# Kernel tuning notes

Measured on AMD Instinct MI355X. Metric: run time of the kernel, lower is better.

Reference implementation:

```python
import jax, jax.numpy as jnp
import numpy as np

B = 128; DIM_IN = 3; MAX_CYCLE = 50; NODES = 18
T = MAX_CYCLE * NODES          # cycle_size = 900
F1, F2 = 32, 64                # stgcn_filters
NCLS = 3
N = B * T                      # nodes seen by GATv2 = 115200
E = 12 * N                     # edges (avg degree 12)
EPS = 1e-5


def setup_inputs() -> dict:
    key = jax.random.key(0)
    keys = iter(jax.random.split(key, 48))
    def p(shape, scale=0.05):
        return jax.random.normal(next(keys), shape, jnp.float32) * scale
    inp = {}
    inp["x"] = jax.random.normal(next(keys), (B, DIM_IN, T), jnp.float32)
    inp["edge_index"] = jax.random.randint(next(keys), (2, E), 0, N)
    def block(pfx, cin, c):
        inp[pfx + "_tc1_w"] = p((c, cin, 5)); inp[pfx + "_tc1_b"] = p((c,))
        inp[pfx + "_wl"] = p((c, c)); inp[pfx + "_bl"] = p((c,))
        inp[pfx + "_wr"] = p((c, c)); inp[pfx + "_br"] = p((c,))
        inp[pfx + "_att"] = p((c,)); inp[pfx + "_gbias"] = p((c,))
        inp[pfx + "_bn_g"] = jnp.ones((c,), jnp.float32)
        inp[pfx + "_bn_b"] = jnp.zeros((c,), jnp.float32)
        inp[pfx + "_tc2_w"] = p((c, c, 5)); inp[pfx + "_tc2_b"] = p((c,))
    block("b1", DIM_IN, F1)
    block("b2", F1, F2)
    inp["fc1_w"] = p((128, T * F2), 0.01); inp["fc1_b"] = p((128,))
    inp["hbn1_g"] = jnp.ones((128,), jnp.float32); inp["hbn1_b"] = jnp.zeros((128,), jnp.float32)
    inp["fc2_w"] = p((64, 128)); inp["fc2_b"] = p((64,))
    inp["hbn2_g"] = jnp.ones((64,), jnp.float32); inp["hbn2_b"] = jnp.zeros((64,), jnp.float32)
    inp["fc3_w"] = p((NCLS, 64)); inp["fc3_b"] = p((NCLS,))
    return inp


def _conv1d_same(x, w, b):
    # x: [B, Cin, T], w: [Cout, Cin, 5], 'same' padding (pad 2/2)
    y = jax.lax.conv_general_dilated(x, w, (1,), [(2, 2)],
                                     dimension_numbers=("NCH", "OIH", "NCH"))
    return y + b[None, :, None]


def _bn(h, g, b):
    # BatchNorm1d on [N, C] with batch statistics
    m = h.mean(0)
    v = h.var(0)
    return (h - m) * jax.lax.rsqrt(v + EPS) * g + b


def _gatv2(h, src, dst, wl, bl, wr, br, att, gbias):
    # PyG GATv2Conv, heads=1, negative_slope=0.2, self loops already in src/dst
    xl = h @ wl.T + bl            # source transform, also the message
    xr = h @ wr.T + br            # target transform
    e = jnp.dot(jax.nn.leaky_relu(xl[src] + xr[dst], 0.2), att)  # [E]
    m = jax.ops.segment_max(e, dst, num_segments=N)
    ex = jnp.exp(e - m[dst])
    s = jax.ops.segment_sum(ex, dst, num_segments=N)
    alpha = ex / s[dst]
    out = jax.ops.segment_sum(alpha[:, None] * xl[src], dst, num_segments=N)
    return out + gbias


def _block(x, src, dst, tc1_w, tc1_b, wl, bl, wr, br, att, gbias, bn_g, bn_b, tc2_w, tc2_b):
    x = jax.nn.relu(_conv1d_same(x, tc1_w, tc1_b))      # [B, C, T]
    C = tc1_w.shape[0]
    h = x.reshape(T * B, C)                             # torch .view(T*B, C) (raw row-major)
    h = jax.nn.relu(_gatv2(h, src, dst, wl, bl, wr, br, att, gbias))
    h = _bn(h, bn_g, bn_b)
    h = h.reshape(B, C, T)                              # torch .view(B, C, T)
    return jax.nn.relu(_conv1d_same(h, tc2_w, tc2_b))


def reference(x, edge_index,
              b1_tc1_w, b1_tc1_b, b1_wl, b1_bl, b1_wr, b1_br, b1_att, b1_gbias,
              b1_bn_g, b1_bn_b, b1_tc2_w, b1_tc2_b,
              b2_tc1_w, b2_tc1_b, b2_wl, b2_bl, b2_wr, b2_br, b2_att, b2_gbias,
              b2_bn_g, b2_bn_b, b2_tc2_w, b2_tc2_b,
              fc1_w, fc1_b, hbn1_g, hbn1_b, fc2_w, fc2_b, hbn2_g, hbn2_b, fc3_w, fc3_b):
    sl = jnp.arange(N, dtype=edge_index.dtype)          # PyG add_self_loops=True
    src = jnp.concatenate([edge_index[0], sl])
    dst = jnp.concatenate([edge_index[1], sl])
    h = _block(x, src, dst, b1_tc1_w, b1_tc1_b, b1_wl, b1_bl, b1_wr, b1_br,
               b1_att, b1_gbias, b1_bn_g, b1_bn_b, b1_tc2_w, b1_tc2_b)
    h = jax.nn.relu(h)                                  # extra relu on non-final block (dropout off)
    h = _block(h, src, dst, b2_tc1_w, b2_tc1_b, b2_wl, b2_bl, b2_wr, b2_br,
               b2_att, b2_gbias, b2_bn_g, b2_bn_b, b2_tc2_w, b2_tc2_b)
    h = h.reshape(B, F2 * T)
    h = jax.nn.relu(h @ fc1_w.T + fc1_b)
    h = _bn(h, hbn1_g, hbn1_b)
    h = jax.nn.relu(h @ fc2_w.T + fc2_b)
    h = _bn(h, hbn2_g, hbn2_b)
    logits = h @ fc3_w.T + fc3_b
    return (jax.nn.sigmoid(logits), logits)
```

## Files before the change

kernel.cpp:

```cpp
#include <hip/hip_runtime.h>
#include <hip/hip_bf16.h>

typedef __hip_bfloat16 bf16;
typedef __attribute__((ext_vector_type(8))) short s16x8;
typedef __attribute__((ext_vector_type(4))) float f32x4;
#define DEV static __device__ __forceinline__

DEV float b2f(bf16 v){ return __bfloat162float(v); }
DEV bf16  f2b(float v){ return __float2bfloat16(v); }
DEV int   is_f32(const void* gones){ return ((const unsigned int*)gones)[0] == 0x3F800000u ? 1 : 0; }
DEV float ldin(const void* p, int f32, int i){
    return f32 ? ((const float*)p)[i] : __bfloat162float(((const bf16*)p)[i]);
}
DEV void unpk(unsigned u, float& a, float& b){
    a = __uint_as_float(u << 16);
    b = __uint_as_float(u & 0xffff0000u);
}
DEV float lrelu(float t){ return fmaxf(t, 0.f) + 0.2f * fminf(t, 0.f); }
DEV unsigned short bfu(float v){ bf16 h = f2b(v); return *(unsigned short*)&h; }

constexpr int Bb  = 128;
constexpr int Tt  = 900;
constexpr int Nn  = Bb * Tt;
constexpr int Ee  = 12 * Nn;
constexpr int CAP = 48;
constexpr int NBK  = 256;
constexpr int NPB  = Nn / NBK;
constexpr int BCAP = 8192;
constexpr int WROWS = 96 + 1024 + 2048 + 4096;
constexpr int WTOT  = WROWS * 5;
constexpr int WBF   = 5120 + 10240 + 20480;
constexpr int WXT   = 2*32*32 + 64 + 2*64*64 + 128;

__global__ __launch_bounds__(256) void k_wprep(const void* wa, const void* wb_, const void* wc,
    const void* wd,
    const void* b1wl, const void* b1bl, const void* b1wr, const void* b1br,
    const void* b2wl, const void* b2bl, const void* b2wr, const void* b2br,
    const void* gones, float* __restrict__ wp, bf16* __restrict__ wbf,
    float* __restrict__ wx, int* __restrict__ gcur){
    const int f32 = is_f32(gones);
    if (blockIdx.x == 0 && threadIdx.x < NBK) gcur[threadIdx.x] = 0;
    int e = blockIdx.x * 256 + threadIdx.x;
    if (e < WTOT){
        int r = e / 5, k = e - r * 5;
        const void* src; int rb;
        if (r < 96)      { src = wa; rb = 0; }
        else if (r < 1120){ src = wb_; rb = 96; }
        else if (r < 3168){ src = wc; rb = 1120; }
        else             { src = wd; rb = 3168; }
        wp[r * 8 + k] = ldin(src, f32, (r - rb) * 5 + k);
    } else if (e < WTOT + WBF){
        int e2 = e - WTOT;
        const void* src; int kk, r;
        if (e2 < 5120)      { kk = e2 >> 10; r = e2 & 1023; src = wb_; }
        else if (e2 < 15360){ int e3 = e2 - 5120;  kk = e3 >> 11; r = e3 & 2047; src = wc; }
        else                { int e3 = e2 - 15360; kk = e3 >> 12; r = e3 & 4095; src = wd; }
        wbf[e2] = f2b(ldin(src, f32, r * 5 + kk));
    } else if (e < WTOT + WBF + WXT){
        int e3 = e - WTOT - WBF;
        float v;
        if      (e3 < 1024){ int t = e3;         int c = t >> 5, f = t & 31; v = ldin(b1wl, f32, f * 32 + c); }
        else if (e3 < 2048){ int t = e3 - 1024;  int c = t >> 5, f = t & 31; v = ldin(b1wr, f32, f * 32 + c); }
        else if (e3 < 2080)  v = ldin(b1bl, f32, e3 - 2048);
        else if (e3 < 2112)  v = ldin(b1br, f32, e3 - 2080);
        else if (e3 < 6208){ int t = e3 - 2112;  int c = t >> 6, f = t & 63; v = ldin(b2wl, f32, f * 64 + c); }
        else if (e3 < 10304){int t = e3 - 6208;  int c = t >> 6, f = t & 63; v = ldin(b2wr, f32, f * 64 + c); }
        else if (e3 < 10368) v = ldin(b2bl, f32, e3 - 10304);
        else                 v = ldin(b2br, f32, e3 - 10368);
        wx[e3] = v;
    }
}

__global__ __launch_bounds__(256) void k_bucket(const int* __restrict__ ei,
                                                int* __restrict__ gcur, int2* __restrict__ bkt){
    constexpr int TILE = 4096;
    const int base = blockIdx.x * TILE;
    const int tid = threadIdx.x;
    __shared__ int cnt[NBK];
    __shared__ int gbase[NBK];
    cnt[tid] = 0;
    __syncthreads();
    int es[16], er[16], eb[16], rk[16];
    #pragma unroll
    for (int k = 0; k < 16; ++k){
        int idx = base + k * 256 + tid;
        if (idx < Ee){
            es[k] = ei[idx];
            int d = ei[Ee + idx];
            eb[k] = d / NPB;
            er[k] = d - eb[k] * NPB;
            rk[k] = atomicAdd(&cnt[eb[k]], 1);
        } else eb[k] = -1;
    }
    __syncthreads();
    {
        int c = cnt[tid];
        gbase[tid] = (c > 0) ? atomicAdd(&gcur[tid], c) : 0;
    }
    __syncthreads();
    #pragma unroll
    for (int k = 0; k < 16; ++k){
        if (eb[k] >= 0){
            int slot = gbase[eb[k]] + rk[k];
            if (slot < BCAP)
                bkt[(size_t)eb[k] * BCAP + slot] = make_int2(er[k], es[k]);
        }
    }
}

__global__ __launch_bounds__(256) void k_csr2(const int2* __restrict__ bkt, const int* __restrict__ gcur,
                                              int* __restrict__ csr, int* __restrict__ cnt){
    const int b = blockIdx.x;
    const int n0 = b * NPB;
    __shared__ int lcnt[NPB];
    for (int i = threadIdx.x; i < NPB; i += 256) lcnt[i] = 0;
    __syncthreads();
    const int tot = min(gcur[b], BCAP);
    for (int i = threadIdx.x; i < tot; i += 256){
        int2 e = bkt[(size_t)b * BCAP + i];
        int p = atomicAdd(&lcnt[e.x], 1);
        if (p < CAP) csr[(size_t)(n0 + e.x) * CAP + p] = e.y;
    }
    __syncthreads();
    for (int i = threadIdx.x; i < NPB; i += 256) cnt[n0 + i] = lcnt[i];
}

template<bool EXT, int CIN, int COUT, bool BN>
__global__ __launch_bounds__(256) void k_conv(const void* __restrict__ x,
    const float* __restrict__ wp, int wbase,
    const void* __restrict__ bias, const float* __restrict__ scale, const float* __restrict__ shift,
    const void* __restrict__ gones, float* __restrict__ y)
{
    const int f32 = is_f32(gones);
    __shared__ alignas(16) float xs[CIN][132];
    const int b = blockIdx.x >> 3, t0 = (blockIdx.x & 7) * 128;
    const int tid = threadIdx.x;
    for (int i = tid; i < CIN * 132; i += 256){
        int ci = i / 132, tt = i % 132;
        int gt = t0 + tt - 2;
        float v = 0.f;
        if (gt >= 0 && gt < Tt){
            int idx = (b * CIN + ci) * Tt + gt;
            v = EXT ? ldin(x, f32, idx) : ((const float*)x)[idx];
            if (BN){
                int f = (ci * (Tt % CIN) + gt) % CIN;
                v = v * scale[f] + shift[f];
            }
        }
        xs[ci][tt] = v;
    }
    __syncthreads();
    constexpr int HALF = COUT / 2;
    constexpr int NT   = 256 / HALF;
    constexpr int NW   = 128 / (NT * 4);
    const int cop = tid / NT;
    const int tch = tid % NT;
    const int co = cop, co2 = cop + HALF;
    float acc[NW][2][4];
    #pragma unroll
    for (int iw = 0; iw < NW; ++iw)
        #pragma unroll
        for (int h = 0; h < 2; ++h)
            #pragma unroll
            for (int j = 0; j < 4; ++j) acc[iw][h][j] = 0.f;

    const float* w0p = wp + (size_t)(wbase + co  * CIN) * 8;
    const float* w1p = wp + (size_t)(wbase + co2 * CIN) * 8;
    float4 na = *(const float4*)w0p; float na4 = w0p[4];
    float4 nb = *(const float4*)w1p; float nb4 = w1p[4];
    for (int ci = 0; ci < CIN; ++ci){
        const float w0[5] = {na.x, na.y, na.z, na.w, na4};
        const float w1[5] = {nb.x, nb.y, nb.z, nb.w, nb4};
        if (ci + 1 < CIN){
            const float* p0 = w0p + (size_t)(ci + 1) * 8;
            const float* p1 = w1p + (size_t)(ci + 1) * 8;
            na = *(const float4*)p0; na4 = p0[4];
            nb = *(const float4*)p1; nb4 = p1[4];
        }
        #pragma unroll
        for (int iw = 0; iw < NW; ++iw){
            const int tl = tch * 4 + iw * NT * 4;
            float4 a  = *(const float4*)&xs[ci][tl];
            float4 bq = *(const float4*)&xs[ci][tl + 4];
            float xw[8] = {a.x,a.y,a.z,a.w,bq.x,bq.y,bq.z,bq.w};
            #pragma unroll
            for (int k = 0; k < 5; ++k)
                #pragma unroll
                for (int j = 0; j < 4; ++j){
                    acc[iw][0][j] = fmaf(xw[j + k], w0[k], acc[iw][0][j]);
                    acc[iw][1][j] = fmaf(xw[j + k], w1[k], acc[iw][1][j]);
                }
        }
    }
    const float bv0 = ldin(bias, f32, co), bv1 = ldin(bias, f32, co2);
    #pragma unroll
    for (int iw = 0; iw < NW; ++iw){
        const int t = t0 + tch * 4 + iw * NT * 4;
        if (t < Tt){
            float4 o0, o1;
            o0.x = fmaxf(acc[iw][0][0] + bv0, 0.f); o0.y = fmaxf(acc[iw][0][1] + bv0, 0.f);
            o0.z = fmaxf(acc[iw][0][2] + bv0, 0.f); o0.w = fmaxf(acc[iw][0][3] + bv0, 0.f);
            o1.x = fmaxf(acc[iw][1][0] + bv1, 0.f); o1.y = fmaxf(acc[iw][1][1] + bv1, 0.f);
            o1.z = fmaxf(acc[iw][1][2] + bv1, 0.f); o1.w = fmaxf(acc[iw][1][3] + bv1, 0.f);
            *(float4*)&y[(b * COUT + co ) * Tt + t] = o0;
            *(float4*)&y[(b * COUT + co2) * Tt + t] = o1;
        }
    }
}

template<int CIN, int COUT, bool BN>
__global__ __launch_bounds__(256) void k_convM(const float* __restrict__ x, const bf16* __restrict__ wbf,
    int wbase,
    const void* __restrict__ bias, const float* __restrict__ scale, const float* __restrict__ shift,
    const void* __restrict__ gones, float* __restrict__ y)
{
    const int f32 = is_f32(gones);
    constexpr int STR = CIN + 8;
    constexpr int CI2 = CIN / 2;
    __shared__ alignas(16) float smem[COUT * 132];
    unsigned short* xsT = (unsigned short*)smem;
    const int b = blockIdx.x >> 3, t0 = (blockIdx.x & 7) * 128;
    const int tid = threadIdx.x;
    for (int i = tid; i < CI2 * 128; i += 256){
        int ci2 = i >> 7, tt = i & 127;
        int gt = t0 + tt - 2;
        int ci = ci2 * 2;
        unsigned pack = 0;
        if (gt >= 0 && gt < Tt){
            float v0 = x[(b * CIN + ci) * Tt + gt];
            float v1 = x[(b * CIN + ci + 1) * Tt + gt];
            if (BN){
                int fa = (4 * ci + gt) & (CIN - 1), fb = (4 * ci + 4 + gt) & (CIN - 1);
                v0 = v0 * scale[fa] + shift[fa];
                v1 = v1 * scale[fb] + shift[fb];
            }
            pack = (unsigned)bfu(v0) | ((unsigned)bfu(v1) << 16);
        }
        *(unsigned*)&xsT[tt * STR + ci] = pack;
    }
    if (tid < CI2 * 4){
        int ci2 = tid >> 2, tt = 128 + (tid & 3);
        int gt = t0 + tt - 2;
        int ci = ci2 * 2;
        unsigned pack = 0;
        if (gt < Tt){
            float v0 = x[(b * CIN + ci) * Tt + gt];
            float v1 = x[(b * CIN + ci + 1) * Tt + gt];
            if (BN){
                int fa = (4 * ci + gt) & (CIN - 1), fb = (4 * ci + 4 + gt) & (CIN - 1);
                v0 = v0 * scale[fa] + shift[fa];
                v1 = v1 * scale[fb] + shift[fb];
            }
            pack = (unsigned)bfu(v0) | ((unsigned)bfu(v1) << 16);
        }
        *(unsigned*)&xsT[tt * STR + ci] = pack;
    }
    __syncthreads();
    const int lane = tid & 63, wid = tid >> 6;
    const int l15 = lane & 15, quad = lane >> 4;
    constexpr int MT  = COUT / 16;
    constexpr int NTP = 2 * MT;
    const int mt  = (MT == 4) ? wid : (wid & 1);
    const int ntb = (MT == 4) ? 0 : (wid >> 1) * NTP;
    const int co0 = mt * 16;
    f32x4 acc[NTP];
    #pragma unroll
    for (int nt = 0; nt < NTP; ++nt){ f32x4 z = {0.f, 0.f, 0.f, 0.f}; acc[nt] = z; }
    for (int kk = 0; kk < 5; ++kk){
        #pragma unroll
        for (int kb = 0; kb < CIN / 32; ++kb){
            s16x8 a = *(const s16x8*)&wbf[wbase + kk * (COUT * CIN) + (co0 + l15) * CIN + kb * 32 + quad * 8];
            #pragma unroll
            for (int nt = 0; nt < NTP; ++nt){
                s16x8 bf = *(const s16x8*)&xsT[((ntb + nt) * 16 + l15 + kk) * STR + kb * 32 + quad * 8];
                acc[nt] = __builtin_amdgcn_mfma_f32_16x16x32_bf16(a, bf, acc[nt], 0, 0, 0);
            }
        }
    }
    __syncthreads();
    #pragma unroll
    for (int nt = 0; nt < NTP; ++nt)
        #pragma unroll
        for (int r = 0; r < 4; ++r)
            smem[(co0 + quad * 4 + r) * 132 + (ntb + nt) * 16 + l15] = acc[nt][r];
    __syncthreads();
    for (int i = tid; i < COUT * 32; i += 256){
        int co = i >> 5, c4 = (i & 31) << 2;
        int t = t0 + c4;
        if (t < Tt){
            float4 o = *(float4*)&smem[co * 132 + c4];
            float bb = ldin(bias, f32, co);
            o.x = fmaxf(o.x + bb, 0.f); o.y = fmaxf(o.y + bb, 0.f);
            o.z = fmaxf(o.z + bb, 0.f); o.w = fmaxf(o.w + bb, 0.f);
            float* dst = &y[(b * COUT + co) * Tt + t];
            if (t + 3 < Tt) *(float4*)dst = o;
            else {
                float ov[4] = {o.x, o.y, o.z, o.w};
                for (int j = 0; j < 4 && t + j < Tt; ++j) dst[j] = ov[j];
            }
        }
    }
}

template<int C>
__global__ __launch_bounds__(256) void k_xlxr(const float* __restrict__ h,
    const float* __restrict__ wx, int wxoff,
    unsigned short* __restrict__ xlh, float* __restrict__ xr)
{
    constexpr int NB = 4096 / C;
    constexpr int HS = NB + 4;
    __shared__ alignas(16) float hT[C][HS];
    __shared__ alignas(16) float wlS[C * C];
    __shared__ alignas(16) float wrS[C * C];
    const int tid = threadIdx.x;
    const int n0 = blockIdx.x * NB;
    for (int i = tid; i < NB * C; i += 256){
        int n = i & (NB - 1), c = i / NB;
        hT[c][n] = h[(size_t)(n0 + n) * C + c];
    }
    const float* wl = wx + wxoff;
    const float* wr = wl + C * C;
    for (int i = tid; i < C * C; i += 256){
        wlS[i] = wl[i];
        wrS[i] = wr[i];
    }
    __syncthreads();
    const float* bl = wr + C * C;
    const float* br = bl + C;
    constexpr int FG = C / 4;
    const int fg = tid % FG, ng = tid / FG;
    const int nloc = ng * 4, floc = fg * 4;
    float blv[4], brv[4];
    #pragma unroll
    for (int j = 0; j < 4; ++j){ blv[j] = bl[floc + j]; brv[j] = br[floc + j]; }
    float accL[4][4], accR[4][4];
    #pragma unroll
    for (int i = 0; i < 4; ++i)
        #pragma unroll
        for (int j = 0; j < 4; ++j){ accL[i][j] = 0.f; accR[i][j] = 0.f; }
    #pragma unroll 4
    for (int c = 0; c < C; ++c){
        float4 hv = *(const float4*)&hT[c][nloc];
        float4 lv = *(const float4*)&wlS[c * C + floc];
        float4 rv = *(const float4*)&wrS[c * C + floc];
        float ha[4] = {hv.x,hv.y,hv.z,hv.w};
        float la[4] = {lv.x,lv.y,lv.z,lv.w};
        float ra[4] = {rv.x,rv.y,rv.z,rv.w};
        #pragma unroll
        for (int i = 0; i < 4; ++i)
            #pragma unroll
            for (int j = 0; j < 4; ++j){
                accL[i][j] = fmaf(ha[i], la[j], accL[i][j]);
                accR[i][j] = fmaf(ha[i], ra[j], accR[i][j]);
            }
    }
    #pragma unroll
    for (int i = 0; i < 4; ++i){
        size_t n = n0 + nloc + i;
        bf16 hb[4];
        hb[0] = f2b(accL[i][0] + blv[0]); hb[1] = f2b(accL[i][1] + blv[1]);
        hb[2] = f2b(accL[i][2] + blv[2]); hb[3] = f2b(accL[i][3] + blv[3]);
        *(ushort4*)&xlh[n * C + floc] = *(ushort4*)hb;
        float4 r;
        r.x = accR[i][0] + brv[0]; r.y = accR[i][1] + brv[1];
        r.z = accR[i][2] + brv[2]; r.w = accR[i][3] + brv[3];
        *(float4*)&xr[n * C + floc] = r;
    }
}

template<int L> DEV float rsumL(float v){
    #pragma unroll
    for (int s = L / 2; s > 0; s >>= 1) v += __shfl_xor(v, s, 64);
    return v;
}

template<int C, int FPL>
__global__ __launch_bounds__(256) void k_gat(const unsigned short* __restrict__ xlh,
    const float* __restrict__ xr,
    const int* __restrict__ csr, const int* __restrict__ cnt,
    const void* __restrict__ att, const void* __restrict__ gbias,
    const void* __restrict__ gones, float* __restrict__ out)
{
    const int f32 = is_f32(gones);
    constexpr int L   = C / FPL;
    constexpr int NPW = 64 / L;
    const int lane = threadIdx.x & 63, wid = threadIdx.x >> 6;
    const int sub = lane / L, fp = lane % L;
    const int node = (blockIdx.x * 4 + wid) * NPW + sub;
    const int f0 = FPL * fp;
    float xrv[FPL], attv[FPL];
    if constexpr (FPL == 4){
        float4 t = *(const float4*)&xr[(size_t)node * C + f0];
        xrv[0] = t.x; xrv[1] = t.y; xrv[2] = t.z; xrv[3] = t.w;
    } else {
        float2 t = *(const float2*)&xr[(size_t)node * C + f0];
        xrv[0] = t.x; xrv[1] = t.y;
    }
    #pragma unroll
    for (int i = 0; i < FPL; ++i) attv[i] = ldin(att, f32, f0 + i);
    const int deg = min(cnt[node], CAP);
    int degu = deg;
    degu = max(degu, __shfl_xor(degu, 32, 64));
    degu = max(degu, __shfl_xor(degu, 16, 64));

    auto loadv = [&](int s, float (&v)[FPL]){
        if constexpr (FPL == 4){
            uint2 u = *(const uint2*)&xlh[(size_t)s * C + f0];
            unpk(u.x, v[0], v[1]); unpk(u.y, v[2], v[3]);
        } else {
            unsigned u = *(const unsigned*)&xlh[(size_t)s * C + f0];
            unpk(u, v[0], v[1]);
        }
    };
    auto score = [&](const float (&v)[FPL]){
        float l = lrelu(v[0] + xrv[0]) * attv[0];
        #pragma unroll
        for (int i = 1; i < FPL; ++i) l = fmaf(lrelu(v[i] + xrv[i]), attv[i], l);
        return rsumL<L>(l);
    };

    float ssum, acc[FPL];
    {
        float v[FPL];
        loadv(node, v);
        float w = __expf(score(v));
        ssum = w;
        #pragma unroll
        for (int i = 0; i < FPL; ++i) acc[i] = w * v[i];
    }
    for (int j = 0; j < degu; j += 4){
        int4 s4 = *(const int4*)&csr[(size_t)node * CAP + j];
        const bool a0 = (j + 0 < deg), a1 = (j + 1 < deg), a2 = (j + 2 < deg), a3 = (j + 3 < deg);
        int s0 = a0 ? s4.x : node, s1 = a1 ? s4.y : node;
        int s2 = a2 ? s4.z : node, s3 = a3 ? s4.w : node;
        float v0[FPL], v1[FPL], v2[FPL], v3[FPL];
        loadv(s0, v0); loadv(s1, v1); loadv(s2, v2); loadv(s3, v3);
        float e0 = score(v0), e1 = score(v1), e2 = score(v2), e3 = score(v3);
        float w0 = a0 ? __expf(e0) : 0.f;
        float w1 = a1 ? __expf(e1) : 0.f;
        float w2 = a2 ? __expf(e2) : 0.f;
        float w3 = a3 ? __expf(e3) : 0.f;
        ssum += (w0 + w1) + (w2 + w3);
        #pragma unroll
        for (int i = 0; i < FPL; ++i)
            acc[i] += fmaf(w0, v0[i], w1 * v1[i]) + fmaf(w2, v2[i], w3 * v3[i]);
    }
    float inv = 1.f / ssum;
    if constexpr (FPL == 4){
        float4 o;
        o.x = fmaxf(fmaf(acc[0], inv, ldin(gbias, f32, f0)),     0.f);
        o.y = fmaxf(fmaf(acc[1], inv, ldin(gbias, f32, f0 + 1)), 0.f);
        o.z = fmaxf(fmaf(acc[2], inv, ldin(gbias, f32, f0 + 2)), 0.f);
        o.w = fmaxf(fmaf(acc[3], inv, ldin(gbias, f32, f0 + 3)), 0.f);
        *(float4*)&out[(size_t)node * C + f0] = o;
    } else {
        float2 o;
        o.x = fmaxf(fmaf(acc[0], inv, ldin(gbias, f32, f0)),     0.f);
        o.y = fmaxf(fmaf(acc[1], inv, ldin(gbias, f32, f0 + 1)), 0.f);
        *(float2*)&out[(size_t)node * C + f0] = o;
    }
}

template<int C>
__global__ __launch_bounds__(256) void k_bnstat1(const float* __restrict__ h, double* __restrict__ part){
    const int tid = threadIdx.x;
    double s1 = 0.0, s2 = 0.0;
    const int total = Nn * C;
    for (int idx = blockIdx.x * 256 + tid; idx < total; idx += 65536){
        float v = h[idx];
        s1 += v; s2 += (double)v * v;
    }
    __shared__ double r1[256], r2[256];
    r1[tid] = s1; r2[tid] = s2;
    __syncthreads();
    if (tid < C){
        double a = 0.0, b = 0.0;
        #pragma unroll
        for (int q = 0; q < 256 / C; ++q){ a += r1[tid + q * C]; b += r2[tid + q * C]; }
        part[blockIdx.x * 2 * C + tid]     = a;
        part[blockIdx.x * 2 * C + C + tid] = b;
    }
}

template<int C>
__global__ void k_bnstat2(const double* __restrict__ part, const void* __restrict__ g,
                          const void* __restrict__ b, const void* __restrict__ gones,
                          float* __restrict__ scale, float* __restrict__ shift){
    const int f32 = is_f32(gones);
    const int f = threadIdx.x;
    double s1 = 0.0, s2 = 0.0;
    for (int s = 0; s < 256; ++s){ s1 += part[s * 2 * C + f]; s2 += part[s * 2 * C + C + f]; }
    double mean = s1 / (double)Nn;
    double var  = s2 / (double)Nn - mean * mean;
    float sc = (float)((double)ldin(g, f32, f) / sqrt(var + 1e-5));
    float sh = ldin(b, f32, f) - (float)mean * sc;
    scale[f] = sc; shift[f] = sh;
}

__global__ __launch_bounds__(256) void k_fc1(const float* __restrict__ h, const void* __restrict__ w1,
                                             const void* __restrict__ gones, float* __restrict__ part){
    const int f32 = is_f32(gones);
    __shared__ alignas(16) float AT[32][136];
    __shared__ alignas(16) float BT[32][136];
    const int tid = threadIdx.x;
    const int blk = blockIdx.x;
    const int k0 = blk * 128;
    const int bg = tid >> 4, jg = tid & 15;
    const int row = tid >> 5, kk = tid & 31;
    float ar[16], br[16];
    #pragma unroll
    for (int q = 0; q < 16; ++q){
        int idx = (row + q * 8) * 57600 + k0 + kk;
        ar[q] = h[idx];
        br[q] = ldin(w1, f32, idx);
    }
    float acc[8][8];
    #pragma unroll
    for (int i = 0; i < 8; ++i)
        #pragma unroll
        for (int j = 0; j < 8; ++j) acc[i][j] = 0.f;
    for (int ch = 0; ch < 4; ++ch){
        __syncthreads();
        #pragma unroll
        for (int q = 0; q < 16; ++q){
            AT[kk][row + q * 8] = ar[q];
            BT[kk][row + q * 8] = br[q];
        }
        __syncthreads();
        if (ch < 3){
            const int kb = k0 + (ch + 1) * 32;
            #pragma unroll
            for (int q = 0; q < 16; ++q){
                int idx = (row + q * 8) * 57600 + kb + kk;
                ar[q] = h[idx];
                br[q] = ldin(w1, f32, idx);
            }
        }
        for (int k2 = 0; k2 < 32; ++k2){
            float4 a0 = *(const float4*)&AT[k2][bg * 8];
            float4 a1 = *(const float4*)&AT[k2][bg * 8 + 4];
            float4 c0 = *(const float4*)&BT[k2][jg * 8];
            float4 c1 = *(const float4*)&BT[k2][jg * 8 + 4];
            float av[8] = {a0.x,a0.y,a0.z,a0.w,a1.x,a1.y,a1.z,a1.w};
            float bv[8] = {c0.x,c0.y,c0.z,c0.w,c1.x,c1.y,c1.z,c1.w};
            #pragma unroll
            for (int i = 0; i < 8; ++i)
                #pragma unroll
                for (int j = 0; j < 8; ++j) acc[i][j] = fmaf(av[i], bv[j], acc[i][j]);
        }
    }
    #pragma unroll
    for (int i = 0; i < 8; ++i){
        int bb = bg * 8 + i;
        #pragma unroll
        for (int q = 0; q < 2; ++q){
            float4 o;
            o.x = acc[i][q*4+0]; o.y = acc[i][q*4+1]; o.z = acc[i][q*4+2]; o.w = acc[i][q*4+3];
            *(float4*)&part[blk * 16384 + bb * 128 + jg * 8 + q * 4] = o;
        }
    }
}

__global__ void k_fc1red1(const float* __restrict__ part, float* __restrict__ pr2){
    const int y = blockIdx.x >> 6;
    const int o = (blockIdx.x & 63) * 256 + threadIdx.x;
    const int sb0 = y * 57;
    const int sb1 = min(sb0 + 57, 450);
    float s = 0.f;
    for (int sb = sb0; sb < sb1; ++sb) s += part[(size_t)sb * 16384 + o];
    pr2[(size_t)y * 16384 + o] = s;
}

__global__ void k_fc1red2(const float* __restrict__ pr2, const void* __restrict__ bias,
                          const void* __restrict__ gones, float* __restrict__ out1){
    const int f32 = is_f32(gones);
    const int o = blockIdx.x * 256 + threadIdx.x;
    float s = ldin(bias, f32, o & 127);
    #pragma unroll
    for (int y = 0; y < 8; ++y) s += pr2[(size_t)y * 16384 + o];
    out1[o] = fmaxf(s, 0.f);
}

__global__ void k_hstat(const float* __restrict__ out1, const void* __restrict__ g1,
                        const void* __restrict__ b1, const void* __restrict__ gones,
                        float* __restrict__ sc, float* __restrict__ sh){
    const int f32 = is_f32(gones);
    const int f = threadIdx.x;
    double s1 = 0.0, s2 = 0.0;
    for (int r = 0; r < 128; ++r){ float v = out1[r * 128 + f]; s1 += v; s2 += (double)v * v; }
    double mean = s1 / 128.0, var = s2 / 128.0 - mean * mean;
    float s = (float)((double)ldin(g1, f32, f) / sqrt(var + 1e-5));
    sc[f] = s;
    sh[f] = ldin(b1, f32, f) - (float)mean * s;
}

__global__ __launch_bounds__(256) void k_fc2(const float* __restrict__ out1,
    const float* __restrict__ sc, const float* __restrict__ sh,
    const void* __restrict__ w2, const void* __restrict__ fb2,
    const void* __restrict__ gones, float* __restrict__ f2)
{
    const int f32 = is_f32(gones);
    __shared__ alignas(16) float hs[4 * 128];
    __shared__ alignas(16) float w2s[64 * 132];
    const int tid = threadIdx.x;
    const int b0 = blockIdx.x * 4;
    for (int i = tid; i < 512; i += 256){
        int f = i & 127;
        hs[i] = out1[b0 * 128 + i] * sc[f] + sh[f];
    }
    for (int i = tid; i < 8192; i += 256)
        w2s[(i >> 7) * 132 + (i & 127)] = ldin(w2, f32, i);
    __syncthreads();
    const int b = tid >> 6, o = tid & 63;
    float acc = ldin(fb2, f32, o);
    const float* hp = &hs[b * 128];
    const float* wq = &w2s[o * 132];
    #pragma unroll
    for (int k = 0; k < 128; k += 4){
        float4 hv = *(const float4*)&hp[k];
        float4 wv = *(const float4*)&wq[k];
        acc = fmaf(hv.x, wv.x, acc); acc = fmaf(hv.y, wv.y, acc);
        acc = fmaf(hv.z, wv.z, acc); acc = fmaf(hv.w, wv.w, acc);
    }
    f2[(b0 + b) * 64 + o] = fmaxf(acc, 0.f);
}

__global__ __launch_bounds__(256) void k_head2(const float* __restrict__ f2,
    const void* g2, const void* b2v, const void* w3, const void* fb3,
    const void* gones, void* __restrict__ out)
{
    const int f32 = is_f32(gones);
    __shared__ float fs[8192];
    __shared__ float sc2[64], sh2[64];
    const int tid = threadIdx.x;
    for (int i = tid; i < 8192; i += 256) fs[i] = f2[i];
    __syncthreads();
    if (tid < 64){
        double s1 = 0.0, s2 = 0.0;
        for (int r = 0; r < 128; ++r){ float v = fs[r * 64 + tid]; s1 += v; s2 += (double)v * v; }
        double mean = s1 / 128.0, var = s2 / 128.0 - mean * mean;
        sc2[tid] = (float)((double)ldin(g2, f32, tid) / sqrt(var + 1e-5));
        sh2[tid] = ldin(b2v, f32, tid) - (float)mean * sc2[tid];
    }
    __syncthreads();
    if (tid < 128){
        float hv[64];
        for (int k = 0; k < 64; ++k) hv[k] = fs[tid * 64 + k] * sc2[k] + sh2[k];
        #pragma unroll
        for (int c = 0; c < 3; ++c){
            float acc = ldin(fb3, f32, c);
            for (int k = 0; k < 64; ++k) acc = fmaf(hv[k], ldin(w3, f32, c * 64 + k), acc);
            float sg = 1.f / (1.f + __expf(-acc));
            if (f32){
                ((float*)out)[384 + tid * 3 + c] = acc;
                ((float*)out)[tid * 3 + c] = sg;
            } else {
                ((bf16*)out)[384 + tid * 3 + c] = f2b(acc);
                ((bf16*)out)[tid * 3 + c] = f2b(sg);
            }
        }
    }
}

extern "C" void kernel_launch(void* const* d_in, const int* in_sizes, int n_in,
                              void* d_out, int out_size, void* d_ws, size_t ws_size,
                              hipStream_t stream)
{
    const void* x   = d_in[0];
    const int*  ei  = (const int*)d_in[1];
    const void* b1_tc1_w=d_in[2];  const void* b1_tc1_b=d_in[3];
    const void* b1_wl   =d_in[4];  const void* b1_bl   =d_in[5];
    const void* b1_wr   =d_in[6];  const void* b1_br   =d_in[7];
    const void* b1_att  =d_in[8];  const void* b1_gb   =d_in[9];
    const void* b1_g    =d_in[10]; const void* b1_bt   =d_in[11];
    const void* b1_tc2_w=d_in[12]; const void* b1_tc2_b=d_in[13];
    const void* b2_tc1_w=d_in[14]; const void* b2_tc1_b=d_in[15];
    const void* b2_wl   =d_in[16]; const void* b2_bl   =d_in[17];
    const void* b2_wr   =d_in[18]; const void* b2_br   =d_in[19];
    const void* b2_att  =d_in[20]; const void* b2_gb   =d_in[21];
    const void* b2_g    =d_in[22]; const void* b2_bt   =d_in[23];
    const void* b2_tc2_w=d_in[24]; const void* b2_tc2_b=d_in[25];
    const void* fc1_w=d_in[26]; const void* fc1_b=d_in[27];
    const void* hbn1_g=d_in[28]; const void* hbn1_b=d_in[29];
    const void* fc2_w=d_in[30]; const void* fc2_b=d_in[31];
    const void* hbn2_g=d_in[32]; const void* hbn2_b=d_in[33];
    const void* fc3_w=d_in[34]; const void* fc3_b=d_in[35];
    const void* gones = b1_g;

    float* ws = (float*)d_ws;
    const size_t NC = (size_t)Nn * 64;
    float* buf0 = ws;
    float* buf1 = ws + NC;
    float* buf2 = ws + 2 * NC;
    int*   csr  = (int*)(ws + 3 * NC);
    int*   cnt  = (int*)((char*)csr + (size_t)Nn * CAP * 4);
    double* bnp = (double*)((char*)cnt + (size_t)Nn * 4);
    float* scale = (float*)(bnp + 32768);
    float* shift = scale + 128;
    unsigned short* xlh = (unsigned short*)(shift + 128);
    int*   gcur = (int*)(xlh + (size_t)Nn * 64);
    float* wp   = (float*)(gcur + NBK);
    bf16*  wbf  = (bf16*)(wp + (size_t)WROWS * 8);
    float* wx   = (float*)(wbf + WBF);
    int2*  bkt  = (int2*)buf2;
    float* part = buf0;
    float* out1 = buf2;
    float* pr2  = buf2 + 16384;
    float* f2b_ = pr2 + 8 * 16384;
    float* hsc  = f2b_ + 8192;
    float* hsh  = hsc + 128;

    k_wprep <<<(WTOT + WBF + WXT + 255) / 256, 256, 0, stream>>>(
        b1_tc1_w, b1_tc2_w, b2_tc1_w, b2_tc2_w,
        b1_wl, b1_bl, b1_wr, b1_br, b2_wl, b2_bl, b2_wr, b2_br,
        gones, wp, wbf, wx, gcur);
    k_bucket<<<(Ee + 4095) / 4096, 256, 0, stream>>>(ei, gcur, bkt);
    k_csr2  <<<NBK, 256, 0, stream>>>(bkt, gcur, csr, cnt);

    k_conv<true, 3, 32, false><<<Bb * 8, 256, 0, stream>>>(x, wp, 0, b1_tc1_b, nullptr, nullptr, gones, buf0);
    k_xlxr<32><<<Nn / 128, 256, 0, stream>>>(buf0, wx, 0, xlh, buf1);
    k_gat<32, 2><<<Nn / 16, 256, 0, stream>>>(xlh, buf1, csr, cnt, b1_att, b1_gb, gones, buf2);
    k_bnstat1<32><<<256, 256, 0, stream>>>(buf2, bnp);
    k_bnstat2<32><<<1, 32, 0, stream>>>(bnp, b1_g, b1_bt, gones, scale, shift);
    k_convM<32, 32, true><<<Bb * 8, 256, 0, stream>>>(buf2, wbf, 0, b1_tc2_b, scale, shift, gones, buf0);

    k_convM<32, 64, false><<<Bb * 8, 256, 0, stream>>>(buf0, wbf, 5120, b2_tc1_b, nullptr, nullptr, gones, buf1);
    k_xlxr<64><<<Nn / 64, 256, 0, stream>>>(buf1, wx, 2112, xlh, buf2);
    k_gat<64, 4><<<Nn / 16, 256, 0, stream>>>(xlh, buf2, csr, cnt, b2_att, b2_gb, gones, buf0);
    k_bnstat1<64><<<256, 256, 0, stream>>>(buf0, bnp);
    k_bnstat2<64><<<1, 64, 0, stream>>>(bnp, b2_g, b2_bt, gones, scale, shift);
    k_convM<64, 64, true><<<Bb * 8, 256, 0, stream>>>(buf0, wbf, 15360, b2_tc2_b, scale, shift, gones, buf1);

    k_fc1<<<450, 256, 0, stream>>>(buf1, fc1_w, gones, part);
    k_fc1red1<<<512, 256, 0, stream>>>(part, pr2);
    k_fc1red2<<<64, 256, 0, stream>>>(pr2, fc1_b, gones, out1);
    k_hstat<<<1, 128, 0, stream>>>(out1, hbn1_g, hbn1_b, gones, hsc, hsh);
    k_fc2<<<32, 256, 0, stream>>>(out1, hsc, hsh, fc2_w, fc2_b, gones, f2b_);
    k_head2<<<1, 256, 0, stream>>>(f2b_, hbn2_g, hbn2_b, fc3_w, fc3_b, gones, d_out);
}
```

Before: 522.6 us.

## Sort GAT nodes by degree within windows and simplify leaky-relu scoring

Result: no change. 526.1 us (+0.7%).

```diff
diff --git a/kernel.cpp b/kernel.cpp
--- a/kernel.cpp
+++ b/kernel.cpp
@@ -125,6 +125,24 @@
     for (int i = threadIdx.x; i < NPB; i += 256) cnt[n0 + i] = lcnt[i];
 }
 
+__global__ __launch_bounds__(256) void k_dwin(const int* __restrict__ cnt, int* __restrict__ order){
+    __shared__ int hist[CAP + 1];
+    __shared__ int base[CAP + 1];
+    const int n0 = blockIdx.x * 256;
+    const int tid = threadIdx.x;
+    if (tid <= CAP) hist[tid] = 0;
+    __syncthreads();
+    const int d = min(cnt[n0 + tid], CAP);
+    const int r = atomicAdd(&hist[d], 1);
+    __syncthreads();
+    if (tid == 0){
+        int s = 0;
+        for (int i = 0; i <= CAP; ++i){ base[i] = s; s += hist[i]; }
+    }
+    __syncthreads();
+    order[n0 + base[d] + r] = n0 + tid;
+}
+
 template<bool EXT, int CIN, int COUT, bool BN>
 __global__ __launch_bounds__(256) void k_conv(const void* __restrict__ x,
     const float* __restrict__ wp, int wbase,
@@ -378,6 +396,7 @@
 __global__ __launch_bounds__(256) void k_gat(const unsigned short* __restrict__ xlh,
     const float* __restrict__ xr,
     const int* __restrict__ csr, const int* __restrict__ cnt,
+    const int* __restrict__ order,
     const void* __restrict__ att, const void* __restrict__ gbias,
     const void* __restrict__ gones, float* __restrict__ out)
 {
@@ -386,9 +405,9 @@
     constexpr int NPW = 64 / L;
     const int lane = threadIdx.x & 63, wid = threadIdx.x >> 6;
     const int sub = lane / L, fp = lane % L;
-    const int node = (blockIdx.x * 4 + wid) * NPW + sub;
+    const int node = order[(blockIdx.x * 4 + wid) * NPW + sub];
     const int f0 = FPL * fp;
-    float xrv[FPL], attv[FPL];
+    float xrv[FPL], a1v[FPL], a2v[FPL];
     if constexpr (FPL == 4){
         float4 t = *(const float4*)&xr[(size_t)node * C + f0];
         xrv[0] = t.x; xrv[1] = t.y; xrv[2] = t.z; xrv[3] = t.w;
@@ -397,7 +416,11 @@
         xrv[0] = t.x; xrv[1] = t.y;
     }
     #pragma unroll
-    for (int i = 0; i < FPL; ++i) attv[i] = ldin(att, f32, f0 + i);
+    for (int i = 0; i < FPL; ++i){
+        float a = ldin(att, f32, f0 + i);
+        a1v[i] = 0.6f * a;
+        a2v[i] = 0.4f * a;
+    }
     const int deg = min(cnt[node], CAP);
     int degu = deg;
     degu = max(degu, __shfl_xor(degu, 32, 64));
@@ -413,9 +436,13 @@
         }
     };
     auto score = [&](const float (&v)[FPL]){
-        float l = lrelu(v[0] + xrv[0]) * attv[0];
-        #pragma unroll
-        for (int i = 1; i < FPL; ++i) l = fmaf(lrelu(v[i] + xrv[i]), attv[i], l);
+        float l = 0.f;
+        #pragma unroll
+        for (int i = 0; i < FPL; ++i){
+            float t = v[i] + xrv[i];
+            l = fmaf(a1v[i], t, l);
+            l = fmaf(a2v[i], fabsf(t), l);
+        }
         return rsumL<L>(l);
     };
 
@@ -702,6 +729,7 @@
     float* wp   = (float*)(gcur + NBK);
     bf16*  wbf  = (bf16*)(wp + (size_t)WROWS * 8);
     float* wx   = (float*)(wbf + WBF);
+    int*   order = (int*)(wx + WXT);
     int2*  bkt  = (int2*)buf2;
     float* part = buf0;
     float* out1 = buf2;
@@ -716,17 +744,18 @@
         gones, wp, wbf, wx, gcur);
     k_bucket<<<(Ee + 4095) / 4096, 256, 0, stream>>>(ei, gcur, bkt);
     k_csr2  <<<NBK, 256, 0, stream>>>(bkt, gcur, csr, cnt);
+    k_dwin  <<<Nn / 256, 256, 0, stream>>>(cnt, order);
 
     k_conv<true, 3, 32, false><<<Bb * 8, 256, 0, stream>>>(x, wp, 0, b1_tc1_b, nullptr, nullptr, gones, buf0);
     k_xlxr<32><<<Nn / 128, 256, 0, stream>>>(buf0, wx, 0, xlh, buf1);
-    k_gat<32, 2><<<Nn / 16, 256, 0, stream>>>(xlh, buf1, csr, cnt, b1_att, b1_gb, gones, buf2);
+    k_gat<32, 2><<<Nn / 16, 256, 0, stream>>>(xlh, buf1, csr, cnt, order, b1_att, b1_gb, gones, buf2);
     k_bnstat1<32><<<256, 256, 0, stream>>>(buf2, bnp);
     k_bnstat2<32><<<1, 32, 0, stream>>>(bnp, b1_g, b1_bt, gones, scale, shift);
     k_convM<32, 32, true><<<Bb * 8, 256, 0, stream>>>(buf2, wbf, 0, b1_tc2_b, scale, shift, gones, buf0);
 
     k_convM<32, 64, false><<<Bb * 8, 256, 0, stream>>>(buf0, wbf, 5120, b2_tc1_b, nullptr, nullptr, gones, buf1);
     k_xlxr<64><<<Nn / 64, 256, 0, stream>>>(buf1, wx, 2112, xlh, buf2);
-    k_gat<64, 4><<<Nn / 16, 256, 0, stream>>>(xlh, buf2, csr, cnt, b2_att, b2_gb, gones, buf0);
+    k_gat<64, 4><<<Nn / 16, 256, 0, stream>>>(xlh, buf2, csr, cnt, order, b2_att, b2_gb, gones, buf0);
     k_bnstat1<64><<<256, 256, 0, stream>>>(buf0, bnp);
     k_bnstat2<64><<<1, 64, 0, stream>>>(bnp, b2_g, b2_bt, gones, scale, shift);
     k_convM<64, 64, true><<<Bb * 8, 256, 0, stream>>>(buf0, wbf, 15360, b2_tc2_b, scale, shift, gones, buf1);
```
